# Performance work log

Measured on AMD Instinct MI355X. Metric: run time of the kernel, lower is better.

Reference implementation:

```python
import jax, jax.numpy as jnp
import numpy as np

B, N, DIM, H, DH, MLP, DEPTH = 32, 256, 384, 6, 64, 1536, 12
INNER = H * DH
LN_EPS = 1e-5
LS_INIT = 0.1  # LayerScale init_eps for depth <= 18


def setup_inputs() -> dict:
    key = jax.random.key(0)
    ks = jax.random.split(key, 10)
    f = lambda k, shape, s=0.02: jax.random.normal(k, shape, jnp.float32) * s
    return {
        "x": jax.random.normal(ks[0], (B, N, DIM), jnp.float32),
        "ln1_g": jnp.ones((DEPTH, DIM), jnp.float32),
        "ln1_b": jnp.zeros((DEPTH, DIM), jnp.float32),
        "wq": f(ks[1], (DEPTH, DIM, INNER)),
        "wkv": f(ks[2], (DEPTH, DIM, 2 * INNER)),
        "scale": jnp.full((DEPTH, H), DH ** -0.5, jnp.float32),  # learned per-head scale
        "mix_pre": f(ks[3], (DEPTH, H, H), 1.0),   # torch.randn init
        "mix_post": f(ks[4], (DEPTH, H, H), 1.0),
        "wo": f(ks[5], (DEPTH, INNER, DIM)),
        "bo": jnp.zeros((DEPTH, DIM), jnp.float32),
        "ls1": jnp.full((DEPTH, DIM), LS_INIT, jnp.float32),
        "ln2_g": jnp.ones((DEPTH, DIM), jnp.float32),
        "ln2_b": jnp.zeros((DEPTH, DIM), jnp.float32),
        "w1": f(ks[6], (DEPTH, DIM, MLP)),
        "b1": jnp.zeros((DEPTH, MLP), jnp.float32),
        "w2": f(ks[7], (DEPTH, MLP, DIM)),
        "b2": jnp.zeros((DEPTH, DIM), jnp.float32),
        "ls2": jnp.full((DEPTH, DIM), LS_INIT, jnp.float32),
    }


def _layernorm(x, g, b):
    mu = jnp.mean(x, axis=-1, keepdims=True)
    var = jnp.mean(jnp.square(x - mu), axis=-1, keepdims=True)
    return (x - mu) * jax.lax.rsqrt(var + LN_EPS) * g + b


def reference(x, ln1_g, ln1_b, wq, wkv, scale, mix_pre, mix_post, wo, bo, ls1,
              ln2_g, ln2_b, w1, b1, w2, b2, ls2):
    diag = jnp.eye(N, dtype=bool)  # self-attention diagonal mask

    def block(x, p):
        (g1, bb1, wq_, wkv_, sc, mp, mq, wo_, bo_, l1,
         g2, bb2, w1_, b1_, w2_, b2_, l2) = p
        # --- talking-heads attention (PreNorm + LayerScale + residual) ---
        y = _layernorm(x, g1, bb1)
        q = (y @ wq_).reshape(B, N, H, DH).transpose(0, 2, 1, 3)       # b h n d
        kv = y @ wkv_
        k, v = jnp.split(kv, 2, axis=-1)
        k = k.reshape(B, N, H, DH).transpose(0, 2, 1, 3)
        v = v.reshape(B, N, H, DH).transpose(0, 2, 1, 3)
        dots = jnp.einsum('bhid,bhjd->bhij', q, k) * sc[None, :, None, None]
        dots = jnp.einsum('bhij,hg->bgij', dots, mp)                   # pre-softmax head mix
        dots = jnp.where(diag, -jnp.inf, dots)                         # mask self positions
        attn = jax.nn.softmax(dots, axis=-1)
        attn = jnp.einsum('bhij,hg->bgij', attn, mq)                   # post-softmax head mix
        o = jnp.einsum('bhij,bhjd->bhid', attn, v)
        o = o.transpose(0, 2, 1, 3).reshape(B, N, INNER) @ wo_ + bo_
        x = o * l1 + x
        # --- FFN (PreNorm + LayerScale + residual) ---
        y2 = _layernorm(x, g2, bb2)
        h = jax.nn.gelu(y2 @ w1_ + b1_, approximate=False)
        x = (h @ w2_ + b2_) * l2 + x
        return x, None

    params = (ln1_g, ln1_b, wq, wkv, scale, mix_pre, mix_post, wo, bo, ls1,
              ln2_g, ln2_b, w1, b1, w2, b2, ls2)
    x, _ = jax.lax.scan(block, x, params)
    return x
```

## Files before the change

### kernel.cpp

```cpp
#include <hip/hip_runtime.h>
#include <hip/hip_bf16.h>
#include <math.h>

#define B_ 32
#define N_ 256
#define DIM_ 384
#define H_ 6
#define DH_ 64
#define INNER_ 384
#define MLP_ 1536
#define DEPTH_ 12
#define T_ (B_ * N_)

typedef __bf16 bf16x8 __attribute__((ext_vector_type(8)));
typedef __bf16 bf16x4 __attribute__((ext_vector_type(4)));
typedef float f32x4 __attribute__((ext_vector_type(4)));

#define WQKV_OFF 0
#define WO_OFF   (1152 * 384)
#define W1_OFF   (WO_OFF + 384 * 384)
#define W2_OFF   (W1_OFF + 1536 * 384)
#define WBUF_ELEMS (W2_OFF + 384 * 1536)

__global__ __launch_bounds__(256) void convert_w(
    const float* __restrict__ wq, const float* __restrict__ wkv,
    const float* __restrict__ wo, const float* __restrict__ w1,
    const float* __restrict__ w2, __bf16* __restrict__ wbuf)
{
    __shared__ float til[64][65];
    int t = blockIdx.x;
    int lane = threadIdx.x & 63, seg = threadIdx.x >> 6;
    const float* src; __bf16* dst;
    int Ns, sc, dK, dR, k0;
    if (t < 108) {
        int nt = t / 6, kt = t % 6;
        int n0 = nt * 64; k0 = kt * 64;
        dst = wbuf + WQKV_OFF; dK = 384; dR = n0;
        if (n0 < 384) { src = wq;  Ns = 384; sc = n0; }
        else          { src = wkv; Ns = 768; sc = n0 - 384; }
    } else if (t < 144) {
        int u = t - 108; int nt = u / 6, kt = u % 6;
        src = wo; Ns = 384; sc = nt * 64;
        dst = wbuf + WO_OFF; dK = 384; dR = nt * 64; k0 = kt * 64;
    } else if (t < 288) {
        int u = t - 144; int nt = u / 6, kt = u % 6;
        src = w1; Ns = 1536; sc = nt * 64;
        dst = wbuf + W1_OFF; dK = 384; dR = nt * 64; k0 = kt * 64;
    } else {
        int u = t - 288; int nt = u / 24, kt = u % 24;
        src = w2; Ns = 384; sc = nt * 64;
        dst = wbuf + W2_OFF; dK = 1536; dR = nt * 64; k0 = kt * 64;
    }
    #pragma unroll
    for (int r = 0; r < 16; ++r) {
        int i = seg * 16 + r;
        til[i][lane] = src[(size_t)(k0 + i) * Ns + sc + lane];
    }
    __syncthreads();
    #pragma unroll
    for (int r = 0; r < 16; ++r) {
        int i = seg * 16 + r;
        dst[(size_t)(dR + i) * dK + k0 + lane] = (__bf16)til[lane][i];
    }
}

__global__ __launch_bounds__(64) void ln1w(
    const float* __restrict__ x, const float* __restrict__ g,
    const float* __restrict__ b, __bf16* __restrict__ y)
{
    size_t row = blockIdx.x;
    int lane = threadIdx.x;
    const float* xr = x + row * DIM_;
    float v[6];
    #pragma unroll
    for (int s = 0; s < 6; ++s) v[s] = xr[lane + 64 * s];
    float sum = 0.f;
    #pragma unroll
    for (int s = 0; s < 6; ++s) sum += v[s];
    #pragma unroll
    for (int o = 32; o > 0; o >>= 1) sum += __shfl_xor(sum, o);
    float mu = sum * (1.0f / DIM_);
    float var = 0.f;
    #pragma unroll
    for (int s = 0; s < 6; ++s) { float d = v[s] - mu; var += d * d; }
    #pragma unroll
    for (int o = 32; o > 0; o >>= 1) var += __shfl_xor(var, o);
    float rs = rsqrtf(var * (1.0f / DIM_) + 1e-5f);
    __bf16* yr = y + row * DIM_;
    #pragma unroll
    for (int s = 0; s < 6; ++s) {
        int e = lane + 64 * s;
        yr[e] = (__bf16)((v[s] - mu) * rs * g[e] + b[e]);
    }
}

#define LDK 40

template<int MODE, int K>
__global__ __launch_bounds__(256) void gemm128(
    const __bf16* __restrict__ A, const __bf16* __restrict__ Bt,
    const float* __restrict__ bias, const float* __restrict__ ls,
    float* __restrict__ xf, __bf16* __restrict__ out,
    __bf16* __restrict__ oq, __bf16* __restrict__ ok, __bf16* __restrict__ ov,
    int Nn)
{
    __shared__ __bf16 sA[2][128 * LDK];
    __shared__ __bf16 sB[2][128 * LDK];
    int id = blockIdx.x;
    int g = id & 7, j = id >> 3;
    int bm = (g + ((j & 7) << 3)) << 7;
    int bn = (j >> 3) << 7;
    int tid = threadIdx.x;
    int lane = tid & 63, wid = tid >> 6;
    int wm = (wid & 1) * 64, wn = (wid >> 1) * 64;
    int fm = lane & 15, fq = lane >> 4;

    f32x4 acc[4][4] = {};

    int sr = tid >> 1, sh = (tid & 1) << 4;
    const __bf16* aSrc = A + (size_t)(bm + sr) * K + sh;
    const __bf16* bSrc = Bt + (size_t)(bn + sr) * K + sh;
    int soff = sr * LDK + sh;

    constexpr int nIter = K >> 5;

    {
        bf16x8 a0 = *(const bf16x8*)(aSrc);
        bf16x8 a1 = *(const bf16x8*)(aSrc + 8);
        bf16x8 b0 = *(const bf16x8*)(bSrc);
        bf16x8 b1 = *(const bf16x8*)(bSrc + 8);
        *(bf16x8*)&sA[0][soff]     = a0;
        *(bf16x8*)&sA[0][soff + 8] = a1;
        *(bf16x8*)&sB[0][soff]     = b0;
        *(bf16x8*)&sB[0][soff + 8] = b1;
    }
    bf16x8 pa0 = *(const bf16x8*)(aSrc + 32);
    bf16x8 pa1 = *(const bf16x8*)(aSrc + 40);
    bf16x8 pb0 = *(const bf16x8*)(bSrc + 32);
    bf16x8 pb1 = *(const bf16x8*)(bSrc + 40);
    __syncthreads();

    #pragma unroll
    for (int i = 0; i < nIter; ++i) {
        int cur = i & 1, nxt = cur ^ 1;
        bf16x8 af[4], bf[4];
        #pragma unroll
        for (int ii = 0; ii < 4; ++ii)
            af[ii] = *(const bf16x8*)&sA[cur][(wm + ii * 16 + fm) * LDK + fq * 8];
        #pragma unroll
        for (int jj = 0; jj < 4; ++jj)
            bf[jj] = *(const bf16x8*)&sB[cur][(wn + jj * 16 + fm) * LDK + fq * 8];
        if (i + 1 < nIter) {
            *(bf16x8*)&sA[nxt][soff]     = pa0;
            *(bf16x8*)&sA[nxt][soff + 8] = pa1;
            *(bf16x8*)&sB[nxt][soff]     = pb0;
            *(bf16x8*)&sB[nxt][soff + 8] = pb1;
        }
        if (i + 2 < nIter) {
            int ko = (i + 2) << 5;
            pa0 = *(const bf16x8*)(aSrc + ko);
            pa1 = *(const bf16x8*)(aSrc + ko + 8);
            pb0 = *(const bf16x8*)(bSrc + ko);
            pb1 = *(const bf16x8*)(bSrc + ko + 8);
        }
        #pragma unroll
        for (int ii = 0; ii < 4; ++ii)
            #pragma unroll
            for (int jj = 0; jj < 4; ++jj)
                acc[ii][jj] = __builtin_amdgcn_mfma_f32_16x16x32_bf16(af[ii], bf[jj], acc[ii][jj], 0, 0, 0);
        if (i + 1 < nIter) __syncthreads();
    }

    #pragma unroll
    for (int jj = 0; jj < 4; ++jj) {
        int col = bn + wn + jj * 16 + fm;
        float bv = (MODE != 0) ? bias[col] : 0.0f;
        float lv = (MODE == 2) ? ls[col] : 0.0f;
        #pragma unroll
        for (int i = 0; i < 4; ++i) {
            #pragma unroll
            for (int r = 0; r < 4; ++r) {
                int row = bm + wm + i * 16 + fq * 4 + r;
                float v = acc[i][jj][r];
                if (MODE == 0) {
                    if (col < 384)      oq[(size_t)row * 384 + col] = (__bf16)v;
                    else if (col < 768) ok[(size_t)row * 384 + col - 384] = (__bf16)v;
                    else {
                        int bb = row >> 8, tj = row & 255;
                        ov[((size_t)bb * 384 + (col - 768)) * 256 + tj] = (__bf16)v;
                    }
                } else if (MODE == 1) {
                    v += bv;
                    v = 0.5f * v * (1.0f + erff(v * 0.70710678118f));
                    out[(size_t)row * Nn + col] = (__bf16)v;
                } else {
                    size_t idx = (size_t)row * Nn + col;
                    xf[idx] = (v + bv) * lv + xf[idx];
                }
            }
        }
    }
}

#define PAD_S 264

__global__ __launch_bounds__(384) void attn_mfma(
    const __bf16* __restrict__ q, const __bf16* __restrict__ kb,
    const __bf16* __restrict__ vT, const float* __restrict__ scale,
    const float* __restrict__ mp, const float* __restrict__ mq,
    __bf16* __restrict__ o)
{
    __shared__ __bf16 sbuf[96][PAD_S];
    __shared__ float smp[36], smq[36];

    int id = blockIdx.x;
    int b = (id & 7) + ((id >> 3) & 3) * 8;
    int i0 = (id >> 5) * 16;
    int tid = threadIdx.x;
    int lane = tid & 63, wid = tid >> 6;
    int fm = lane & 15, fq = lane >> 4;

    if (tid < 36) {
        smp[tid] = mp[tid] * scale[tid / 6];
        smq[tid] = mq[tid];
    }

    int h = wid;
    bf16x8 qf[2];
    #pragma unroll
    for (int ks = 0; ks < 2; ++ks)
        qf[ks] = *(const bf16x8*)&q[(size_t)(b * 256 + i0 + fm) * 384 + h * 64 + ks * 32 + fq * 8];
    #pragma unroll 4
    for (int jt = 0; jt < 16; ++jt) {
        f32x4 a = {};
        #pragma unroll
        for (int ks = 0; ks < 2; ++ks) {
            bf16x8 bf = *(const bf16x8*)&kb[(size_t)(b * 256 + jt * 16 + fm) * 384 + h * 64 + ks * 32 + fq * 8];
            a = __builtin_amdgcn_mfma_f32_16x16x32_bf16(qf[ks], bf, a, 0, 0, 0);
        }
        #pragma unroll
        for (int r = 0; r < 4; ++r)
            sbuf[h * 16 + fq * 4 + r][jt * 16 + fm] = (__bf16)a[r];
    }
    __syncthreads();

    for (int idx = tid; idx < 4096; idx += 384) {
        int qq = idx >> 8, jx = idx & 255;
        float sv[6], ovv[6];
        #pragma unroll
        for (int h2 = 0; h2 < 6; ++h2) sv[h2] = (float)sbuf[h2 * 16 + qq][jx];
        #pragma unroll
        for (int gg = 0; gg < 6; ++gg) {
            float r2 = 0.f;
            #pragma unroll
            for (int h2 = 0; h2 < 6; ++h2) r2 += sv[h2] * smp[h2 * 6 + gg];
            ovv[gg] = (jx == i0 + qq) ? -1e30f : r2;
        }
        #pragma unroll
        for (int gg = 0; gg < 6; ++gg) sbuf[gg * 16 + qq][jx] = (__bf16)ovv[gg];
    }
    __syncthreads();

    for (int rr = 0; rr < 16; ++rr) {
        int row = wid * 16 + rr;
        bf16x4 v4 = *(const bf16x4*)&sbuf[row][lane * 4];
        float v0 = (float)v4[0], v1 = (float)v4[1], v2 = (float)v4[2], v3 = (float)v4[3];
        float m = fmaxf(fmaxf(v0, v1), fmaxf(v2, v3));
        #pragma unroll
        for (int off = 32; off > 0; off >>= 1) m = fmaxf(m, __shfl_xor(m, off));
        float e0 = __expf(v0 - m), e1 = __expf(v1 - m), e2 = __expf(v2 - m), e3 = __expf(v3 - m);
        float s = e0 + e1 + e2 + e3;
        #pragma unroll
        for (int off = 32; off > 0; off >>= 1) s += __shfl_xor(s, off);
        float inv = 1.0f / s;
        bf16x4 w4 = { (__bf16)(e0 * inv), (__bf16)(e1 * inv), (__bf16)(e2 * inv), (__bf16)(e3 * inv) };
        *(bf16x4*)&sbuf[row][lane * 4] = w4;
    }
    __syncthreads();

    for (int idx = tid; idx < 4096; idx += 384) {
        int qq = idx >> 8, jx = idx & 255;
        float sv[6], ovv[6];
        #pragma unroll
        for (int h2 = 0; h2 < 6; ++h2) sv[h2] = (float)sbuf[h2 * 16 + qq][jx];
        #pragma unroll
        for (int gg = 0; gg < 6; ++gg) {
            float r2 = 0.f;
            #pragma unroll
            for (int h2 = 0; h2 < 6; ++h2) r2 += sv[h2] * smq[h2 * 6 + gg];
            ovv[gg] = r2;
        }
        #pragma unroll
        for (int gg = 0; gg < 6; ++gg) sbuf[gg * 16 + qq][jx] = (__bf16)ovv[gg];
    }
    __syncthreads();

    int gg = wid;
    f32x4 acco[4] = {};
    #pragma unroll
    for (int jc = 0; jc < 4; ++jc) {
        #pragma unroll
        for (int ks = 0; ks < 2; ++ks) {
            bf16x8 af = *(const bf16x8*)&sbuf[gg * 16 + fm][jc * 64 + ks * 32 + fq * 8];
            #pragma unroll
            for (int nt = 0; nt < 4; ++nt) {
                bf16x8 bf = *(const bf16x8*)&vT[(size_t)(b * 384 + gg * 64 + nt * 16 + fm) * 256 + jc * 64 + ks * 32 + fq * 8];
                acco[nt] = __builtin_amdgcn_mfma_f32_16x16x32_bf16(af, bf, acco[nt], 0, 0, 0);
            }
        }
    }
    #pragma unroll
    for (int nt = 0; nt < 4; ++nt)
        #pragma unroll
        for (int r = 0; r < 4; ++r)
            o[(size_t)(b * 256 + i0 + fq * 4 + r) * 384 + gg * 64 + nt * 16 + fm] = (__bf16)acco[nt][r];
}

extern "C" void kernel_launch(void* const* d_in, const int* in_sizes, int n_in,
                              void* d_out, int out_size, void* d_ws, size_t ws_size,
                              hipStream_t stream) {
    const float* x      = (const float*)d_in[0];
    const float* ln1_g  = (const float*)d_in[1];
    const float* ln1_b  = (const float*)d_in[2];
    const float* wq     = (const float*)d_in[3];
    const float* wkv    = (const float*)d_in[4];
    const float* scale  = (const float*)d_in[5];
    const float* mixp   = (const float*)d_in[6];
    const float* mixq   = (const float*)d_in[7];
    const float* wo     = (const float*)d_in[8];
    const float* bo     = (const float*)d_in[9];
    const float* ls1    = (const float*)d_in[10];
    const float* ln2_g  = (const float*)d_in[11];
    const float* ln2_b  = (const float*)d_in[12];
    const float* w1     = (const float*)d_in[13];
    const float* b1     = (const float*)d_in[14];
    const float* w2     = (const float*)d_in[15];
    const float* b2     = (const float*)d_in[16];
    const float* ls2    = (const float*)d_in[17];

    char* ws = (char*)d_ws;
    float*  xf = (float*)ws;                      ws += (size_t)T_ * DIM_ * 4;
    __bf16* y  = (__bf16*)ws;                     ws += (size_t)T_ * DIM_ * 2;
    __bf16* q  = (__bf16*)ws;                     ws += (size_t)T_ * DIM_ * 2;
    __bf16* kb = (__bf16*)ws;                     ws += (size_t)T_ * DIM_ * 2;
    __bf16* vT = (__bf16*)ws;                     ws += (size_t)T_ * DIM_ * 2;
    __bf16* o  = (__bf16*)ws;                     ws += (size_t)T_ * DIM_ * 2;
    __bf16* wbuf = (__bf16*)ws;                   ws += (size_t)WBUF_ELEMS * 2;
    __bf16* h  = q;

    size_t nBytes = (size_t)T_ * DIM_ * sizeof(float);
    hipMemcpyAsync(xf, x, nBytes, hipMemcpyDeviceToDevice, stream);

    for (int l = 0; l < DEPTH_; ++l) {
        convert_w<<<432, 256, 0, stream>>>(
            wq + (size_t)l * DIM_ * INNER_, wkv + (size_t)l * DIM_ * 2 * INNER_,
            wo + (size_t)l * INNER_ * DIM_, w1 + (size_t)l * DIM_ * MLP_,
            w2 + (size_t)l * MLP_ * DIM_, wbuf);

        ln1w<<<T_, 64, 0, stream>>>(xf, ln1_g + (size_t)l * DIM_, ln1_b + (size_t)l * DIM_, y);

        gemm128<0, 384><<<64 * 9, 256, 0, stream>>>(
            y, wbuf + WQKV_OFF, nullptr, nullptr, nullptr, nullptr,
            q, kb, vT, 1152);

        attn_mfma<<<512, 384, 0, stream>>>(
            q, kb, vT, scale + (size_t)l * H_,
            mixp + (size_t)l * H_ * H_, mixq + (size_t)l * H_ * H_, o);

        gemm128<2, 384><<<64 * 3, 256, 0, stream>>>(
            o, wbuf + WO_OFF, bo + (size_t)l * DIM_, ls1 + (size_t)l * DIM_,
            xf, nullptr, nullptr, nullptr, nullptr, DIM_);

        ln1w<<<T_, 64, 0, stream>>>(xf, ln2_g + (size_t)l * DIM_, ln2_b + (size_t)l * DIM_, y);

        gemm128<1, 384><<<64 * 12, 256, 0, stream>>>(
            y, wbuf + W1_OFF, b1 + (size_t)l * MLP_, nullptr,
            nullptr, h, nullptr, nullptr, nullptr, MLP_);

        gemm128<2, 1536><<<64 * 3, 256, 0, stream>>>(
            h, wbuf + W2_OFF, b2 + (size_t)l * DIM_, ls2 + (size_t)l * DIM_,
            xf, nullptr, nullptr, nullptr, nullptr, DIM_);
    }

    hipMemcpyAsync(d_out, xf, nBytes, hipMemcpyDeviceToDevice, stream);
}
```

Before: 2.008 ms.

## Fuse pre-mix, masked softmax and post-mix into one register pass

Replaces the three separate shared-memory passes (pre-softmax head mix, row softmax, post-softmax head mix), each followed by a barrier, with one pass. In it each wave loads a query row for all six heads into registers, mixes, masks and softmaxes them, then applies the post mix before a single write back. The mixing matrices now live in per-thread registers, loaded from global memory, instead of shared memory. This removes two barriers and two LDS round trips with bf16 rounding between stages. The cost is higher register pressure (72 mix coefficients plus 48 values per thread) and a poor load balance, because only 16 rows are spread over 6 waves.

```diff
diff --git a/kernel.cpp b/kernel.cpp
--- a/kernel.cpp
+++ b/kernel.cpp
@@ -211,7 +211,6 @@
     __bf16* __restrict__ o)
 {
     __shared__ __bf16 sbuf[96][PAD_S];
-    __shared__ float smp[36], smq[36];
 
     int id = blockIdx.x;
     int b = (id & 7) + ((id >> 3) & 3) * 8;
@@ -220,11 +219,6 @@
     int lane = tid & 63, wid = tid >> 6;
     int fm = lane & 15, fq = lane >> 4;
 
-    if (tid < 36) {
-        smp[tid] = mp[tid] * scale[tid / 6];
-        smq[tid] = mq[tid];
-    }
-
     int h = wid;
     bf16x8 qf[2];
     #pragma unroll
@@ -235,63 +229,64 @@
         f32x4 a = {};
         #pragma unroll
         for (int ks = 0; ks < 2; ++ks) {
-            bf16x8 bf = *(const bf16x8*)&kb[(size_t)(b * 256 + jt * 16 + fm) * 384 + h * 64 + ks * 32 + fq * 8];
-            a = __builtin_amdgcn_mfma_f32_16x16x32_bf16(qf[ks], bf, a, 0, 0, 0);
+            bf16x8 bfr = *(const bf16x8*)&kb[(size_t)(b * 256 + jt * 16 + fm) * 384 + h * 64 + ks * 32 + fq * 8];
+            a = __builtin_amdgcn_mfma_f32_16x16x32_bf16(qf[ks], bfr, a, 0, 0, 0);
         }
         #pragma unroll
         for (int r = 0; r < 4; ++r)
             sbuf[h * 16 + fq * 4 + r][jt * 16 + fm] = (__bf16)a[r];
     }
+
+    float mps[36], mqs[36];
+    #pragma unroll
+    for (int t = 0; t < 36; ++t) { mps[t] = mp[t] * scale[t / 6]; mqs[t] = mq[t]; }
+
     __syncthreads();
 
-    for (int idx = tid; idx < 4096; idx += 384) {
-        int qq = idx >> 8, jx = idx & 255;
-        float sv[6], ovv[6];
-        #pragma unroll
-        for (int h2 = 0; h2 < 6; ++h2) sv[h2] = (float)sbuf[h2 * 16 + qq][jx];
-        #pragma unroll
-        for (int gg = 0; gg < 6; ++gg) {
-            float r2 = 0.f;
-            #pragma unroll
-            for (int h2 = 0; h2 < 6; ++h2) r2 += sv[h2] * smp[h2 * 6 + gg];
-            ovv[gg] = (jx == i0 + qq) ? -1e30f : r2;
-        }
-        #pragma unroll
-        for (int gg = 0; gg < 6; ++gg) sbuf[gg * 16 + qq][jx] = (__bf16)ovv[gg];
-    }
-    __syncthreads();
-
-    for (int rr = 0; rr < 16; ++rr) {
-        int row = wid * 16 + rr;
-        bf16x4 v4 = *(const bf16x4*)&sbuf[row][lane * 4];
-        float v0 = (float)v4[0], v1 = (float)v4[1], v2 = (float)v4[2], v3 = (float)v4[3];
-        float m = fmaxf(fmaxf(v0, v1), fmaxf(v2, v3));
-        #pragma unroll
-        for (int off = 32; off > 0; off >>= 1) m = fmaxf(m, __shfl_xor(m, off));
-        float e0 = __expf(v0 - m), e1 = __expf(v1 - m), e2 = __expf(v2 - m), e3 = __expf(v3 - m);
-        float s = e0 + e1 + e2 + e3;
-        #pragma unroll
-        for (int off = 32; off > 0; off >>= 1) s += __shfl_xor(s, off);
-        float inv = 1.0f / s;
-        bf16x4 w4 = { (__bf16)(e0 * inv), (__bf16)(e1 * inv), (__bf16)(e2 * inv), (__bf16)(e3 * inv) };
-        *(bf16x4*)&sbuf[row][lane * 4] = w4;
-    }
-    __syncthreads();
-
-    for (int idx = tid; idx < 4096; idx += 384) {
-        int qq = idx >> 8, jx = idx & 255;
-        float sv[6], ovv[6];
-        #pragma unroll
-        for (int h2 = 0; h2 < 6; ++h2) sv[h2] = (float)sbuf[h2 * 16 + qq][jx];
-        #pragma unroll
-        for (int gg = 0; gg < 6; ++gg) {
-            float r2 = 0.f;
-            #pragma unroll
-            for (int h2 = 0; h2 < 6; ++h2) r2 += sv[h2] * smq[h2 * 6 + gg];
-            ovv[gg] = r2;
-        }
-        #pragma unroll
-        for (int gg = 0; gg < 6; ++gg) sbuf[gg * 16 + qq][jx] = (__bf16)ovv[gg];
+    for (int i = wid; i < 16; i += 6) {
+        float sv[6][4];
+        #pragma unroll
+        for (int h2 = 0; h2 < 6; ++h2) {
+            bf16x4 v4 = *(const bf16x4*)&sbuf[h2 * 16 + i][lane * 4];
+            #pragma unroll
+            for (int c = 0; c < 4; ++c) sv[h2][c] = (float)v4[c];
+        }
+        int drow = i0 + i;
+        float pv[6][4];
+        #pragma unroll
+        for (int g2 = 0; g2 < 6; ++g2) {
+            float t0[4];
+            #pragma unroll
+            for (int c = 0; c < 4; ++c) {
+                float r2 = 0.f;
+                #pragma unroll
+                for (int h2 = 0; h2 < 6; ++h2) r2 += sv[h2][c] * mps[h2 * 6 + g2];
+                t0[c] = (lane * 4 + c == drow) ? -1e30f : r2;
+            }
+            float m = fmaxf(fmaxf(t0[0], t0[1]), fmaxf(t0[2], t0[3]));
+            #pragma unroll
+            for (int off = 32; off > 0; off >>= 1) m = fmaxf(m, __shfl_xor(m, off));
+            float e0 = __expf(t0[0] - m), e1 = __expf(t0[1] - m);
+            float e2 = __expf(t0[2] - m), e3 = __expf(t0[3] - m);
+            float s = e0 + e1 + e2 + e3;
+            #pragma unroll
+            for (int off = 32; off > 0; off >>= 1) s += __shfl_xor(s, off);
+            float inv = 1.0f / s;
+            pv[g2][0] = e0 * inv; pv[g2][1] = e1 * inv;
+            pv[g2][2] = e2 * inv; pv[g2][3] = e3 * inv;
+        }
+        #pragma unroll
+        for (int g2 = 0; g2 < 6; ++g2) {
+            bf16x4 w4;
+            #pragma unroll
+            for (int c = 0; c < 4; ++c) {
+                float r2 = 0.f;
+                #pragma unroll
+                for (int h2 = 0; h2 < 6; ++h2) r2 += pv[h2][c] * mqs[h2 * 6 + g2];
+                w4[c] = (__bf16)r2;
+            }
+            *(bf16x4*)&sbuf[g2 * 16 + i][lane * 4] = w4;
+        }
     }
     __syncthreads();
 
@@ -304,8 +299,8 @@
             bf16x8 af = *(const bf16x8*)&sbuf[gg * 16 + fm][jc * 64 + ks * 32 + fq * 8];
             #pragma unroll
             for (int nt = 0; nt < 4; ++nt) {
-                bf16x8 bf = *(const bf16x8*)&vT[(size_t)(b * 384 + gg * 64 + nt * 16 + fm) * 256 + jc * 64 + ks * 32 + fq * 8];
-                acco[nt] = __builtin_amdgcn_mfma_f32_16x16x32_bf16(af, bf, acco[nt], 0, 0, 0);
+                bf16x8 bfr = *(const bf16x8*)&vT[(size_t)(b * 384 + gg * 64 + nt * 16 + fm) * 256 + jc * 64 + ks * 32 + fq * 8];
+                acco[nt] = __builtin_amdgcn_mfma_f32_16x16x32_bf16(af, bfr, acco[nt], 0, 0, 0);
             }
         }
     }
```

Result: slower. 2.188 ms (+9.0%).
